# Optimization experiments

Hardware: AMD Instinct MI355X
Metric: run time of the kernel (lower is better)

Reference implementation:

```python
import jax, jax.numpy as jnp
import numpy as np

N_NODES = 100000
IN_DIM = 128
OUT_DIM = 128


def setup_inputs() -> dict:
    key = jax.random.key(0)
    ks = jax.random.split(key, 10)
    # entry counts must be multiples of the edge arity (shape)
    e1, e2, e3 = 300000, 600000, 600000  # arities 1, 2, 3 -> 300k/300k/200k hyperedges
    return {
        "x": jax.random.normal(ks[0], (N_NODES, IN_DIM), dtype=jnp.float32),
        "edge_idx_r1": jax.random.randint(ks[1], (2, e1), 0, N_NODES, dtype=jnp.int32),
        "edge_idx_r2": jax.random.randint(ks[2], (2, e2), 0, N_NODES, dtype=jnp.int32),
        "edge_idx_r3": jax.random.randint(ks[3], (2, e3), 0, N_NODES, dtype=jnp.int32),
        "A_r1": jax.random.normal(ks[4], (IN_DIM * 1, OUT_DIM), dtype=jnp.float32) * np.sqrt(2.0 / (IN_DIM * 1 + OUT_DIM)),
        "A_r2": jax.random.normal(ks[5], (IN_DIM * 2, OUT_DIM), dtype=jnp.float32) * np.sqrt(2.0 / (IN_DIM * 2 + OUT_DIM)),
        "A_r3": jax.random.normal(ks[6], (IN_DIM * 3, OUT_DIM), dtype=jnp.float32) * np.sqrt(2.0 / (IN_DIM * 3 + OUT_DIM)),
        "C_w": jax.random.normal(ks[7], (OUT_DIM, IN_DIM), dtype=jnp.float32) * (1.0 / np.sqrt(IN_DIM)),
        "C_b": jax.random.normal(ks[8], (OUT_DIM,), dtype=jnp.float32) * 0.01,
    }


def _edge_type_messages(x, edge_idx, A, arity, n_nodes):
    # edge_idx: [2, groups*arity]; row0 = src node ids, row1 reshaped -> dest = col 0
    dest = edge_idx[1].reshape(-1, arity)[:, 0]              # [groups]
    src = x[edge_idx[0]].reshape(-1, x.shape[1] * arity)     # [groups, in_dim*arity]
    msg = src @ A                                            # [groups, out_dim]
    # degree normalization within this edge type (== 1/counts from torch.unique)
    counts = jnp.zeros((n_nodes,), dtype=msg.dtype).at[dest].add(1.0)
    msg = msg * (1.0 / counts[dest])[:, None]
    return dest, msg


def reference(x, edge_idx_r1, edge_idx_r2, edge_idx_r3, A_r1, A_r2, A_r3, C_w, C_b):
    n = x.shape[0]
    agg = jnp.zeros((n, C_w.shape[0]), dtype=x.dtype)
    for ei, A, arity in ((edge_idx_r1, A_r1, 1), (edge_idx_r2, A_r2, 2), (edge_idx_r3, A_r3, 3)):
        dest, msg = _edge_type_messages(x, ei, A, arity, n)
        agg = agg.at[dest].add(msg)
    return x @ C_w.T + C_b + agg
```

## Files before the change

### kernel.cpp

```cpp
#include <hip/hip_runtime.h>

#define N_NODES 100000
#define DIM 128

typedef __attribute__((ext_vector_type(8))) short bf16x8;
typedef __attribute__((ext_vector_type(4))) float f32x4;
typedef __attribute__((ext_vector_type(8))) unsigned short ushort8;

__device__ __forceinline__ unsigned short f2bf(float f) {
    union { float f; unsigned u; } v; v.f = f;
    unsigned u = v.u + 0x7FFFu + ((v.u >> 16) & 1u);
    return (unsigned short)(u >> 16);
}
__device__ __forceinline__ float bl(unsigned u) { return __uint_as_float(u << 16); }
__device__ __forceinline__ float bh(unsigned u) { return __uint_as_float(u & 0xFFFF0000u); }

__device__ __forceinline__ void gload_lds16(const void* g, void* l) {
    __builtin_amdgcn_global_load_lds((const __attribute__((address_space(1))) void*)g,
                                     (__attribute__((address_space(3))) void*)l, 16, 0, 0);
}

__device__ __forceinline__ void acc2(float4& a, uint2 v) {
    a.x += bl(v.x); a.y += bh(v.x); a.z += bl(v.y); a.w += bh(v.y);
}
__device__ __forceinline__ void red4(float4& a) {
    a.x += __shfl_xor(a.x, 32); a.y += __shfl_xor(a.y, 32);
    a.z += __shfl_xor(a.z, 32); a.w += __shfl_xor(a.w, 32);
}
__device__ __forceinline__ uint2 pack4(float4 a) {
    uint2 r;
    r.x = (unsigned)f2bf(a.x) | ((unsigned)f2bf(a.y) << 16);
    r.y = (unsigned)f2bf(a.z) | ((unsigned)f2bf(a.w) << 16);
    return r;
}

__global__ void cvt_count_kernel(const float* __restrict__ x, unsigned short* __restrict__ xb,
                                 int n8, const int* __restrict__ e1d,
                                 const int* __restrict__ e2d, const int* __restrict__ e3d,
                                 int ng1, int ng12, int ngall, int* __restrict__ counts) {
    int i = blockIdx.x * 256 + threadIdx.x;
    if (i < n8) {
        const float4* p = reinterpret_cast<const float4*>(x) + (size_t)i * 2;
        float4 a = p[0], b = p[1];
        ushort8 o;
        o[0] = f2bf(a.x); o[1] = f2bf(a.y); o[2] = f2bf(a.z); o[3] = f2bf(a.w);
        o[4] = f2bf(b.x); o[5] = f2bf(b.y); o[6] = f2bf(b.z); o[7] = f2bf(b.w);
        *reinterpret_cast<ushort8*>(xb + (size_t)i * 8) = o;
    }
    if (i < ng1) atomicAdd(&counts[e1d[i]], 1);
    else if (i < ng12) atomicAdd(&counts[N_NODES + e2d[(size_t)(i - ng1) * 2]], 1);
    else if (i < ngall) atomicAdd(&counts[2 * N_NODES + e3d[(size_t)(i - ng12) * 3]], 1);
}

__global__ void cvt_B_all(const float* __restrict__ A1, const float* __restrict__ A2,
                          const float* __restrict__ A3, const float* __restrict__ Cw,
                          unsigned short* __restrict__ bts) {
    int kg = blockIdx.x;
    int c = threadIdx.x;
    float v;
    int slice, kp;
    if (kg < 128)      { slice = 0; kp = kg; v = A1[(size_t)kg * 128 + c]; }
    else if (kg < 384) { int k = kg - 128; slice = 1 + (k >> 7); kp = k & 127; v = A2[(size_t)k * 128 + c]; }
    else if (kg < 768) { int k = kg - 384; slice = 3 + (k >> 7); kp = k & 127; v = A3[(size_t)k * 128 + c]; }
    else               { int k = kg - 768; slice = 6; kp = k; v = Cw[(size_t)c * 128 + k]; }
    bts[(size_t)slice * 16384 + c * 128 + kp] = f2bf(v);
}

__global__ __launch_bounds__(256) void scan_p1(const int* __restrict__ counts,
                                               int* __restrict__ partials) {
    __shared__ int red[256];
    int type = blockIdx.y, blk = blockIdx.x, tid = threadIdx.x;
    int base = blk * 4096 + tid * 16;
    int s = 0;
#pragma unroll
    for (int j = 0; j < 16; ++j) {
        int i = base + j;
        s += (i < N_NODES) ? counts[(size_t)type * N_NODES + i] : 0;
    }
    red[tid] = s;
    __syncthreads();
    for (int off = 128; off > 0; off >>= 1) {
        if (tid < off) red[tid] += red[tid + off];
        __syncthreads();
    }
    if (tid == 0) partials[type * 32 + blk] = red[0];
}

__global__ __launch_bounds__(256) void scan_p3(const int* __restrict__ counts,
                                               const int* __restrict__ partials,
                                               int* __restrict__ cursor) {
    __shared__ int tsum[256];
    __shared__ int baseoff;
    int type = blockIdx.y, blk = blockIdx.x, tid = threadIdx.x;
    if (tid == 0) {
        int r = 0;
        for (int b = 0; b < blk; ++b) r += partials[type * 32 + b];
        baseoff = r;
    }
    int base = blk * 4096 + tid * 16;
    int v[16];
    int s = 0;
#pragma unroll
    for (int j = 0; j < 16; ++j) {
        int i = base + j;
        v[j] = (i < N_NODES) ? counts[(size_t)type * N_NODES + i] : 0;
        s += v[j];
    }
    tsum[tid] = s;
    __syncthreads();
    for (int off = 1; off < 256; off <<= 1) {
        int t2 = (tid >= off) ? tsum[tid - off] : 0;
        __syncthreads();
        tsum[tid] += t2;
        __syncthreads();
    }
    int run = tsum[tid] - s + baseoff;
#pragma unroll
    for (int j = 0; j < 16; ++j) {
        int i = base + j;
        if (i < N_NODES) cursor[(size_t)type * N_NODES + i] = run;
        run += v[j];
    }
}

__global__ void scatter_all_kernel(const int* __restrict__ e1, const int* __restrict__ e2,
                                   const int* __restrict__ e3, int ne1, int ne2, int ne3,
                                   int ng1, int ng12, int ngall, int* __restrict__ cursor,
                                   int* __restrict__ s1, int2* __restrict__ s2,
                                   int4* __restrict__ s3) {
    int g = blockIdx.x * 256 + threadIdx.x;
    if (g < ng1) {
        int d = e1[ne1 + g];
        s1[atomicAdd(&cursor[d], 1)] = e1[g];
    } else if (g < ng12) {
        int k = g - ng1;
        int d = e2[ne2 + 2 * (size_t)k];
        int2 v; v.x = e2[2 * (size_t)k]; v.y = e2[2 * (size_t)k + 1];
        s2[atomicAdd(&cursor[N_NODES + d], 1)] = v;
    } else if (g < ngall) {
        int k = g - ng12;
        int d = e3[ne3 + 3 * (size_t)k];
        int4 v; v.x = e3[3 * (size_t)k]; v.y = e3[3 * (size_t)k + 1];
        v.z = e3[3 * (size_t)k + 2]; v.w = 0;
        s3[atomicAdd(&cursor[2 * N_NODES + d], 1)] = v;
    }
}

__global__ __launch_bounds__(256) void aggregate_x_kernel(
    const unsigned short* __restrict__ xb,
    const int* __restrict__ s1, const int2* __restrict__ s2, const int4* __restrict__ s3,
    const int* __restrict__ counts, const int* __restrict__ ends,
    unsigned short* __restrict__ gbf)
{
    int d = blockIdx.x * 4 + (threadIdx.x >> 6);
    if (d >= N_NODES) return;
    const int l = threadIdx.x & 63, hw = l >> 5, sl = l & 31;
    float4 a0 = {0,0,0,0}, a1 = {0,0,0,0}, a2 = {0,0,0,0};
    float4 a3 = {0,0,0,0}, a4 = {0,0,0,0}, a5 = {0,0,0,0};

    int c1 = counts[d], c2 = counts[N_NODES + d], c3 = counts[2 * N_NODES + d];
    int e1e = ends[d], e2e = ends[N_NODES + d], e3e = ends[2 * N_NODES + d];

    if (c1) {
        for (int i = e1e - c1 + hw; i < e1e; i += 2) {
            uint2 v = *reinterpret_cast<const uint2*>(xb + (size_t)s1[i] * 128 + sl * 4);
            acc2(a0, v);
        }
        float inv = 1.f / (float)c1;
        a0.x *= inv; a0.y *= inv; a0.z *= inv; a0.w *= inv;
    }
    if (c2) {
        for (int i = e2e - c2 + hw; i < e2e; i += 2) {
            int2 p = s2[i];
            uint2 va = *reinterpret_cast<const uint2*>(xb + (size_t)p.x * 128 + sl * 4);
            uint2 vb = *reinterpret_cast<const uint2*>(xb + (size_t)p.y * 128 + sl * 4);
            acc2(a1, va); acc2(a2, vb);
        }
        float inv = 1.f / (float)c2;
        a1.x *= inv; a1.y *= inv; a1.z *= inv; a1.w *= inv;
        a2.x *= inv; a2.y *= inv; a2.z *= inv; a2.w *= inv;
    }
    if (c3) {
        for (int i = e3e - c3 + hw; i < e3e; i += 2) {
            int4 p = s3[i];
            uint2 va = *reinterpret_cast<const uint2*>(xb + (size_t)p.x * 128 + sl * 4);
            uint2 vb = *reinterpret_cast<const uint2*>(xb + (size_t)p.y * 128 + sl * 4);
            uint2 vc = *reinterpret_cast<const uint2*>(xb + (size_t)p.z * 128 + sl * 4);
            acc2(a3, va); acc2(a4, vb); acc2(a5, vc);
        }
        float inv = 1.f / (float)c3;
        a3.x *= inv; a3.y *= inv; a3.z *= inv; a3.w *= inv;
        a4.x *= inv; a4.y *= inv; a4.z *= inv; a4.w *= inv;
        a5.x *= inv; a5.y *= inv; a5.z *= inv; a5.w *= inv;
    }
    red4(a0); red4(a1); red4(a2); red4(a3); red4(a4); red4(a5);
    if (hw == 0) {
        *reinterpret_cast<uint2*>(gbf + ((size_t)0 * N_NODES + d) * 128 + sl * 4) = pack4(a0);
        *reinterpret_cast<uint2*>(gbf + ((size_t)1 * N_NODES + d) * 128 + sl * 4) = pack4(a1);
        *reinterpret_cast<uint2*>(gbf + ((size_t)2 * N_NODES + d) * 128 + sl * 4) = pack4(a2);
        *reinterpret_cast<uint2*>(gbf + ((size_t)3 * N_NODES + d) * 128 + sl * 4) = pack4(a3);
        *reinterpret_cast<uint2*>(gbf + ((size_t)4 * N_NODES + d) * 128 + sl * 4) = pack4(a4);
        *reinterpret_cast<uint2*>(gbf + ((size_t)5 * N_NODES + d) * 128 + sl * 4) = pack4(a5);
    }
}

__global__ __launch_bounds__(256, 2) void gemm_out_kernel(
    const unsigned short* __restrict__ xb, const unsigned short* __restrict__ gbf,
    const unsigned short* __restrict__ bts, const float* __restrict__ Cb,
    float* __restrict__ out, int nnodes)
{
    __shared__ __align__(16) char smem[65536];

    const int tid = threadIdx.x;
    const int w = tid >> 6, l = tid & 63;
    const int g0 = blockIdx.x * 128;
    const int lrow = l & 15, lk = l >> 4;
    const int wr = (w & 1) * 64, wc = (w >> 1) * 64;

    const int q = (((l & 7) ^ (l >> 3)) << 4);
    const int inner = q & 63;
    const int rpq = ((l >> 3) << 1) + (q >> 6);

    int aoff[4];
#pragma unroll
    for (int mi = 0; mi < 4; ++mi) {
        int r = wr + mi * 16 + lrow;
        int P = r >> 1;
        aoff[mi] = P * 128 + ((((r & 1) << 6) | (lk << 4)) ^ ((P & 7) << 4));
    }

    f32x4 acc[4][4];
#pragma unroll
    for (int mi = 0; mi < 4; ++mi)
#pragma unroll
        for (int ni = 0; ni < 4; ++ni) acc[mi][ni] = (f32x4){0.f, 0.f, 0.f, 0.f};

    auto STAGE = [&](int c, int buf) {
#pragma unroll
        for (int i = 0; i < 2; ++i) {
            int u = w * 2 + i;
            int r = u * 16 + rpq;
            int row = (g0 + r < nnodes) ? g0 + r : 0;
            const char* src = (c < 6)
                ? (const char*)gbf + ((size_t)c * N_NODES + row) * 256
                : (const char*)xb + (size_t)row * 256;
#pragma unroll
            for (int t2 = 0; t2 < 4; ++t2)
                gload_lds16(src + t2 * 64 + inner, smem + buf * 32768 + t2 * 8192 + u * 1024);
        }
    };

    STAGE(0, 0);
    asm volatile("s_waitcnt vmcnt(0)" ::: "memory");
    __builtin_amdgcn_s_barrier();
    asm volatile("" ::: "memory");

    for (int c = 0; c < 7; ++c) {
        if (c + 1 < 7) STAGE(c + 1, (c + 1) & 1);
        const int bb = (c & 1) * 32768;
#pragma unroll
        for (int ks = 0; ks < 4; ++ks) {
            bf16x8 af[4], bg[4];
#pragma unroll
            for (int mi = 0; mi < 4; ++mi)
                af[mi] = *reinterpret_cast<const bf16x8*>(smem + bb + ks * 8192 + aoff[mi]);
#pragma unroll
            for (int ni = 0; ni < 4; ++ni)
                bg[ni] = *reinterpret_cast<const bf16x8*>(
                    bts + (size_t)c * 16384 + (wc + ni * 16 + lrow) * 128 + ks * 32 + lk * 8);
            __builtin_amdgcn_s_setprio(1);
#pragma unroll
            for (int mi = 0; mi < 4; ++mi)
#pragma unroll
                for (int ni = 0; ni < 4; ++ni)
                    acc[mi][ni] = __builtin_amdgcn_mfma_f32_16x16x32_bf16(
                        af[mi], bg[ni], acc[mi][ni], 0, 0, 0);
            __builtin_amdgcn_s_setprio(0);
        }
        asm volatile("s_waitcnt vmcnt(0)" ::: "memory");
        __builtin_amdgcn_s_barrier();
        asm volatile("" ::: "memory");
    }

    float bv[4];
#pragma unroll
    for (int ni = 0; ni < 4; ++ni) bv[ni] = Cb[wc + ni * 16 + lrow];
#pragma unroll
    for (int mi = 0; mi < 4; ++mi)
#pragma unroll
        for (int reg = 0; reg < 4; ++reg) {
            int g = g0 + wr + mi * 16 + lk * 4 + reg;
            if (g < nnodes) {
#pragma unroll
                for (int ni = 0; ni < 4; ++ni)
                    out[(size_t)g * DIM + wc + ni * 16 + lrow] = acc[mi][ni][reg] + bv[ni];
            }
        }
}

extern "C" void kernel_launch(void* const* d_in, const int* in_sizes, int n_in,
                              void* d_out, int out_size, void* d_ws, size_t ws_size,
                              hipStream_t stream) {
    const float* x  = (const float*)d_in[0];
    const int*   e1 = (const int*)d_in[1];
    const int*   e2 = (const int*)d_in[2];
    const int*   e3 = (const int*)d_in[3];
    const float* A1 = (const float*)d_in[4];
    const float* A2 = (const float*)d_in[5];
    const float* A3 = (const float*)d_in[6];
    const float* Cw = (const float*)d_in[7];
    const float* Cb = (const float*)d_in[8];
    float* out = (float*)d_out;

    const int ne1 = in_sizes[1] / 2, ne2 = in_sizes[2] / 2, ne3 = in_sizes[3] / 2;
    const int ng1 = ne1, ng2 = ne2 / 2, ng3 = ne3 / 3;
    const int N = N_NODES;

    int*  counts  = (int*)d_ws;
    int*  cursor  = counts + 3 * N;
    int4* s3      = (int4*)(cursor + 3 * N);
    int2* s2      = (int2*)(s3 + ng3);
    int*  s1      = (int*)(s2 + ng2);
    int*  partials = s1 + ng1;
    unsigned short* bts = (unsigned short*)(partials + 128);
    unsigned short* xb  = bts + 7 * 16384;
    unsigned short* gbf = xb + (size_t)N * 128;

    const int ngall = ng1 + ng2 + ng3;
    const int n8 = N * DIM / 8;

    hipMemsetAsync(counts, 0, (size_t)3 * N * sizeof(int), stream);
    cvt_count_kernel<<<(n8 + 255) / 256, 256, 0, stream>>>(
        x, xb, n8, e1 + ne1, e2 + ne2, e3 + ne3, ng1, ng1 + ng2, ngall, counts);
    cvt_B_all<<<896, 128, 0, stream>>>(A1, A2, A3, Cw, bts);
    scan_p1<<<dim3(25, 3), 256, 0, stream>>>(counts, partials);
    scan_p3<<<dim3(25, 3), 256, 0, stream>>>(counts, partials, cursor);
    scatter_all_kernel<<<(ngall + 255) / 256, 256, 0, stream>>>(
        e1, e2, e3, ne1, ne2, ne3, ng1, ng1 + ng2, ngall, cursor, s1, s2, s3);
    aggregate_x_kernel<<<(N + 3) / 4, 256, 0, stream>>>(
        xb, s1, s2, s3, counts, cursor, gbf);
    gemm_out_kernel<<<(N + 127) / 128, 256, 0, stream>>>(xb, gbf, bts, Cb, out, N);
}
```

Baseline: 263.7 us.

## Merge prep kernels, pre-scale gather indices, unroll aggregation, hoist B fragment loads

The x conversion, edge counting and weight conversion kernels are merged into one launch with block-range dispatch, removing one kernel launch. Scatter now stores source indices pre-shifted into byte offsets, so the aggregation gather skips the per-index multiply. The aggregation loops are unrolled by two to put more independent loads in flight, and the 1/count scaling moves into the final pack. The GEMM loads all B fragments for a chunk up front rather than per k-step, which raises register pressure. The pre-shifted offsets are 32-bit, which holds only while node_count*256 stays below 2^31.

```diff
diff --git a/kernel.cpp b/kernel.cpp
--- a/kernel.cpp
+++ b/kernel.cpp
@@ -27,43 +27,44 @@
     a.x += __shfl_xor(a.x, 32); a.y += __shfl_xor(a.y, 32);
     a.z += __shfl_xor(a.z, 32); a.w += __shfl_xor(a.w, 32);
 }
-__device__ __forceinline__ uint2 pack4(float4 a) {
+__device__ __forceinline__ uint2 pack4s(float4 a, float inv) {
     uint2 r;
-    r.x = (unsigned)f2bf(a.x) | ((unsigned)f2bf(a.y) << 16);
-    r.y = (unsigned)f2bf(a.z) | ((unsigned)f2bf(a.w) << 16);
+    r.x = (unsigned)f2bf(a.x * inv) | ((unsigned)f2bf(a.y * inv) << 16);
+    r.y = (unsigned)f2bf(a.z * inv) | ((unsigned)f2bf(a.w * inv) << 16);
     return r;
 }
 
-__global__ void cvt_count_kernel(const float* __restrict__ x, unsigned short* __restrict__ xb,
-                                 int n8, const int* __restrict__ e1d,
-                                 const int* __restrict__ e2d, const int* __restrict__ e3d,
-                                 int ng1, int ng12, int ngall, int* __restrict__ counts) {
-    int i = blockIdx.x * 256 + threadIdx.x;
-    if (i < n8) {
-        const float4* p = reinterpret_cast<const float4*>(x) + (size_t)i * 2;
-        float4 a = p[0], b = p[1];
-        ushort8 o;
-        o[0] = f2bf(a.x); o[1] = f2bf(a.y); o[2] = f2bf(a.z); o[3] = f2bf(a.w);
-        o[4] = f2bf(b.x); o[5] = f2bf(b.y); o[6] = f2bf(b.z); o[7] = f2bf(b.w);
-        *reinterpret_cast<ushort8*>(xb + (size_t)i * 8) = o;
-    }
-    if (i < ng1) atomicAdd(&counts[e1d[i]], 1);
-    else if (i < ng12) atomicAdd(&counts[N_NODES + e2d[(size_t)(i - ng1) * 2]], 1);
-    else if (i < ngall) atomicAdd(&counts[2 * N_NODES + e3d[(size_t)(i - ng12) * 3]], 1);
-}
-
-__global__ void cvt_B_all(const float* __restrict__ A1, const float* __restrict__ A2,
-                          const float* __restrict__ A3, const float* __restrict__ Cw,
-                          unsigned short* __restrict__ bts) {
-    int kg = blockIdx.x;
-    int c = threadIdx.x;
-    float v;
-    int slice, kp;
-    if (kg < 128)      { slice = 0; kp = kg; v = A1[(size_t)kg * 128 + c]; }
-    else if (kg < 384) { int k = kg - 128; slice = 1 + (k >> 7); kp = k & 127; v = A2[(size_t)k * 128 + c]; }
-    else if (kg < 768) { int k = kg - 384; slice = 3 + (k >> 7); kp = k & 127; v = A3[(size_t)k * 128 + c]; }
-    else               { int k = kg - 768; slice = 6; kp = k; v = Cw[(size_t)c * 128 + k]; }
-    bts[(size_t)slice * 16384 + c * 128 + kp] = f2bf(v);
+__global__ void prep_kernel(const float* __restrict__ x, unsigned short* __restrict__ xb,
+                            int n8, const int* __restrict__ e1d,
+                            const int* __restrict__ e2d, const int* __restrict__ e3d,
+                            int ng1, int ng12, int ngall, int* __restrict__ counts,
+                            const float* __restrict__ A1, const float* __restrict__ A2,
+                            const float* __restrict__ A3, const float* __restrict__ Cw,
+                            unsigned short* __restrict__ bts, int nxblocks) {
+    if ((int)blockIdx.x < nxblocks) {
+        int i = blockIdx.x * 256 + threadIdx.x;
+        if (i < n8) {
+            const float4* p = reinterpret_cast<const float4*>(x) + (size_t)i * 2;
+            float4 a = p[0], b = p[1];
+            ushort8 o;
+            o[0] = f2bf(a.x); o[1] = f2bf(a.y); o[2] = f2bf(a.z); o[3] = f2bf(a.w);
+            o[4] = f2bf(b.x); o[5] = f2bf(b.y); o[6] = f2bf(b.z); o[7] = f2bf(b.w);
+            *reinterpret_cast<ushort8*>(xb + (size_t)i * 8) = o;
+        }
+        if (i < ng1) atomicAdd(&counts[e1d[i]], 1);
+        else if (i < ng12) atomicAdd(&counts[N_NODES + e2d[(size_t)(i - ng1) * 2]], 1);
+        else if (i < ngall) atomicAdd(&counts[2 * N_NODES + e3d[(size_t)(i - ng12) * 3]], 1);
+    } else {
+        int kg = (blockIdx.x - nxblocks) * 2 + (threadIdx.x >> 7);
+        int c = threadIdx.x & 127;
+        float v;
+        int slice, kp;
+        if (kg < 128)      { slice = 0; kp = kg; v = A1[(size_t)kg * 128 + c]; }
+        else if (kg < 384) { int k = kg - 128; slice = 1 + (k >> 7); kp = k & 127; v = A2[(size_t)k * 128 + c]; }
+        else if (kg < 768) { int k = kg - 384; slice = 3 + (k >> 7); kp = k & 127; v = A3[(size_t)k * 128 + c]; }
+        else               { int k = kg - 768; slice = 6; kp = k; v = Cw[(size_t)c * 128 + k]; }
+        bts[(size_t)slice * 16384 + c * 128 + kp] = f2bf(v);
+    }
 }
 
 __global__ __launch_bounds__(256) void scan_p1(const int* __restrict__ counts,
@@ -131,17 +132,17 @@
     int g = blockIdx.x * 256 + threadIdx.x;
     if (g < ng1) {
         int d = e1[ne1 + g];
-        s1[atomicAdd(&cursor[d], 1)] = e1[g];
+        s1[atomicAdd(&cursor[d], 1)] = e1[g] << 8;
     } else if (g < ng12) {
         int k = g - ng1;
         int d = e2[ne2 + 2 * (size_t)k];
-        int2 v; v.x = e2[2 * (size_t)k]; v.y = e2[2 * (size_t)k + 1];
+        int2 v; v.x = e2[2 * (size_t)k] << 8; v.y = e2[2 * (size_t)k + 1] << 8;
         s2[atomicAdd(&cursor[N_NODES + d], 1)] = v;
     } else if (g < ngall) {
         int k = g - ng12;
         int d = e3[ne3 + 3 * (size_t)k];
-        int4 v; v.x = e3[3 * (size_t)k]; v.y = e3[3 * (size_t)k + 1];
-        v.z = e3[3 * (size_t)k + 2]; v.w = 0;
+        int4 v; v.x = e3[3 * (size_t)k] << 8; v.y = e3[3 * (size_t)k + 1] << 8;
+        v.z = e3[3 * (size_t)k + 2] << 8; v.w = 0;
         s3[atomicAdd(&cursor[2 * N_NODES + d], 1)] = v;
     }
 }
@@ -155,52 +156,70 @@
     int d = blockIdx.x * 4 + (threadIdx.x >> 6);
     if (d >= N_NODES) return;
     const int l = threadIdx.x & 63, hw = l >> 5, sl = l & 31;
+    const char* xp = (const char*)xb + sl * 8;
     float4 a0 = {0,0,0,0}, a1 = {0,0,0,0}, a2 = {0,0,0,0};
     float4 a3 = {0,0,0,0}, a4 = {0,0,0,0}, a5 = {0,0,0,0};
 
-    int c1 = counts[d], c2 = counts[N_NODES + d], c3 = counts[2 * N_NODES + d];
-    int e1e = ends[d], e2e = ends[N_NODES + d], e3e = ends[2 * N_NODES + d];
-
-    if (c1) {
-        for (int i = e1e - c1 + hw; i < e1e; i += 2) {
-            uint2 v = *reinterpret_cast<const uint2*>(xb + (size_t)s1[i] * 128 + sl * 4);
-            acc2(a0, v);
-        }
-        float inv = 1.f / (float)c1;
-        a0.x *= inv; a0.y *= inv; a0.z *= inv; a0.w *= inv;
-    }
-    if (c2) {
-        for (int i = e2e - c2 + hw; i < e2e; i += 2) {
+    const int c1 = counts[d], c2 = counts[N_NODES + d], c3 = counts[2 * N_NODES + d];
+    const int E1 = ends[d], E2 = ends[N_NODES + d], E3 = ends[2 * N_NODES + d];
+
+    {
+        int i = E1 - c1 + hw;
+        for (; i + 2 < E1; i += 4) {
+            int o0 = s1[i], o1 = s1[i + 2];
+            uint2 v0 = *reinterpret_cast<const uint2*>(xp + o0);
+            uint2 v1 = *reinterpret_cast<const uint2*>(xp + o1);
+            acc2(a0, v0); acc2(a0, v1);
+        }
+        if (i < E1) acc2(a0, *reinterpret_cast<const uint2*>(xp + s1[i]));
+    }
+    {
+        int i = E2 - c2 + hw;
+        for (; i + 2 < E2; i += 4) {
+            int2 p0 = s2[i], p1 = s2[i + 2];
+            uint2 va0 = *reinterpret_cast<const uint2*>(xp + p0.x);
+            uint2 vb0 = *reinterpret_cast<const uint2*>(xp + p0.y);
+            uint2 va1 = *reinterpret_cast<const uint2*>(xp + p1.x);
+            uint2 vb1 = *reinterpret_cast<const uint2*>(xp + p1.y);
+            acc2(a1, va0); acc2(a2, vb0); acc2(a1, va1); acc2(a2, vb1);
+        }
+        if (i < E2) {
             int2 p = s2[i];
-            uint2 va = *reinterpret_cast<const uint2*>(xb + (size_t)p.x * 128 + sl * 4);
-            uint2 vb = *reinterpret_cast<const uint2*>(xb + (size_t)p.y * 128 + sl * 4);
-            acc2(a1, va); acc2(a2, vb);
-        }
-        float inv = 1.f / (float)c2;
-        a1.x *= inv; a1.y *= inv; a1.z *= inv; a1.w *= inv;
-        a2.x *= inv; a2.y *= inv; a2.z *= inv; a2.w *= inv;
-    }
-    if (c3) {
-        for (int i = e3e - c3 + hw; i < e3e; i += 2) {
+            acc2(a1, *reinterpret_cast<const uint2*>(xp + p.x));
+            acc2(a2, *reinterpret_cast<const uint2*>(xp + p.y));
+        }
+    }
+    {
+        int i = E3 - c3 + hw;
+        for (; i + 2 < E3; i += 4) {
+            int4 p0 = s3[i], p1 = s3[i + 2];
+            uint2 va0 = *reinterpret_cast<const uint2*>(xp + p0.x);
+            uint2 vb0 = *reinterpret_cast<const uint2*>(xp + p0.y);
+            uint2 vc0 = *reinterpret_cast<const uint2*>(xp + p0.z);
+            uint2 va1 = *reinterpret_cast<const uint2*>(xp + p1.x);
+            uint2 vb1 = *reinterpret_cast<const uint2*>(xp + p1.y);
+            uint2 vc1 = *reinterpret_cast<const uint2*>(xp + p1.z);
+            acc2(a3, va0); acc2(a4, vb0); acc2(a5, vc0);
+            acc2(a3, va1); acc2(a4, vb1); acc2(a5, vc1);
+        }
+        if (i < E3) {
             int4 p = s3[i];
-            uint2 va = *reinterpret_cast<const uint2*>(xb + (size_t)p.x * 128 + sl * 4);
-            uint2 vb = *reinterpret_cast<const uint2*>(xb + (size_t)p.y * 128 + sl * 4);
-            uint2 vc = *reinterpret_cast<const uint2*>(xb + (size_t)p.z * 128 + sl * 4);
-            acc2(a3, va); acc2(a4, vb); acc2(a5, vc);
-        }
-        float inv = 1.f / (float)c3;
-        a3.x *= inv; a3.y *= inv; a3.z *= inv; a3.w *= inv;
-        a4.x *= inv; a4.y *= inv; a4.z *= inv; a4.w *= inv;
-        a5.x *= inv; a5.y *= inv; a5.z *= inv; a5.w *= inv;
+            acc2(a3, *reinterpret_cast<const uint2*>(xp + p.x));
+            acc2(a4, *reinterpret_cast<const uint2*>(xp + p.y));
+            acc2(a5, *reinterpret_cast<const uint2*>(xp + p.z));
+        }
     }
     red4(a0); red4(a1); red4(a2); red4(a3); red4(a4); red4(a5);
     if (hw == 0) {
-        *reinterpret_cast<uint2*>(gbf + ((size_t)0 * N_NODES + d) * 128 + sl * 4) = pack4(a0);
-        *reinterpret_cast<uint2*>(gbf + ((size_t)1 * N_NODES + d) * 128 + sl * 4) = pack4(a1);
-        *reinterpret_cast<uint2*>(gbf + ((size_t)2 * N_NODES + d) * 128 + sl * 4) = pack4(a2);
-        *reinterpret_cast<uint2*>(gbf + ((size_t)3 * N_NODES + d) * 128 + sl * 4) = pack4(a3);
-        *reinterpret_cast<uint2*>(gbf + ((size_t)4 * N_NODES + d) * 128 + sl * 4) = pack4(a4);
-        *reinterpret_cast<uint2*>(gbf + ((size_t)5 * N_NODES + d) * 128 + sl * 4) = pack4(a5);
+        const float i1 = c1 ? 1.f / (float)c1 : 0.f;
+        const float i2 = c2 ? 1.f / (float)c2 : 0.f;
+        const float i3 = c3 ? 1.f / (float)c3 : 0.f;
+        *reinterpret_cast<uint2*>(gbf + ((size_t)0 * N_NODES + d) * 128 + sl * 4) = pack4s(a0, i1);
+        *reinterpret_cast<uint2*>(gbf + ((size_t)1 * N_NODES + d) * 128 + sl * 4) = pack4s(a1, i2);
+        *reinterpret_cast<uint2*>(gbf + ((size_t)2 * N_NODES + d) * 128 + sl * 4) = pack4s(a2, i2);
+        *reinterpret_cast<uint2*>(gbf + ((size_t)3 * N_NODES + d) * 128 + sl * 4) = pack4s(a3, i3);
+        *reinterpret_cast<uint2*>(gbf + ((size_t)4 * N_NODES + d) * 128 + sl * 4) = pack4s(a4, i3);
+        *reinterpret_cast<uint2*>(gbf + ((size_t)5 * N_NODES + d) * 128 + sl * 4) = pack4s(a5, i3);
     }
 }
 
@@ -258,23 +277,26 @@
     for (int c = 0; c < 7; ++c) {
         if (c + 1 < 7) STAGE(c + 1, (c + 1) & 1);
         const int bb = (c & 1) * 32768;
+        bf16x8 bgall[4][4];
+#pragma unroll
+        for (int ks = 0; ks < 4; ++ks)
+#pragma unroll
+            for (int ni = 0; ni < 4; ++ni)
+                bgall[ks][ni] = *reinterpret_cast<const bf16x8*>(
+                    bts + (size_t)c * 16384 + (wc + ni * 16 + lrow) * 128 + ks * 32 + lk * 8);
 #pragma unroll
         for (int ks = 0; ks < 4; ++ks) {
-            bf16x8 af[4], bg[4];
+            bf16x8 af[4];
 #pragma unroll
             for (int mi = 0; mi < 4; ++mi)
                 af[mi] = *reinterpret_cast<const bf16x8*>(smem + bb + ks * 8192 + aoff[mi]);
-#pragma unroll
-            for (int ni = 0; ni < 4; ++ni)
-                bg[ni] = *reinterpret_cast<const bf16x8*>(
-                    bts + (size_t)c * 16384 + (wc + ni * 16 + lrow) * 128 + ks * 32 + lk * 8);
             __builtin_amdgcn_s_setprio(1);
 #pragma unroll
             for (int mi = 0; mi < 4; ++mi)
 #pragma unroll
                 for (int ni = 0; ni < 4; ++ni)
                     acc[mi][ni] = __builtin_amdgcn_mfma_f32_16x16x32_bf16(
-                        af[mi], bg[ni], acc[mi][ni], 0, 0, 0);
+                        af[mi], bgall[ks][ni], acc[mi][ni], 0, 0, 0);
             __builtin_amdgcn_s_setprio(0);
         }
         asm volatile("s_waitcnt vmcnt(0)" ::: "memory");
@@ -328,11 +350,12 @@
 
     const int ngall = ng1 + ng2 + ng3;
     const int n8 = N * DIM / 8;
+    const int nxblocks = (n8 + 255) / 256;
 
     hipMemsetAsync(counts, 0, (size_t)3 * N * sizeof(int), stream);
-    cvt_count_kernel<<<(n8 + 255) / 256, 256, 0, stream>>>(
-        x, xb, n8, e1 + ne1, e2 + ne2, e3 + ne3, ng1, ng1 + ng2, ngall, counts);
-    cvt_B_all<<<896, 128, 0, stream>>>(A1, A2, A3, Cw, bts);
+    prep_kernel<<<nxblocks + 448, 256, 0, stream>>>(
+        x, xb, n8, e1 + ne1, e2 + ne2, e3 + ne3, ng1, ng1 + ng2, ngall, counts,
+        A1, A2, A3, Cw, bts, nxblocks);
     scan_p1<<<dim3(25, 3), 256, 0, stream>>>(counts, partials);
     scan_p3<<<dim3(25, 3), 256, 0, stream>>>(counts, partials, cursor);
     scatter_all_kernel<<<(ngall + 255) / 256, 256, 0, stream>>>(
```

Result: no change. 265.8 us (+0.8%).
